# Kernel tuning notes

Hardware: AMD Instinct MI355X
Metric: run time of the kernel (lower is better)

The kernel has to match this reference:

```python
import jax, jax.numpy as jnp
import numpy as np

HEADS_FEAT = 8
HEADS_SAMP = 8
EPS = 1e-5


def _ln(x, g, b):
    m = jnp.mean(x, -1, keepdims=True)
    v = jnp.mean((x - m) ** 2, -1, keepdims=True)
    return (x - m) * jax.lax.rsqrt(v + EPS) * g + b


def _mha(q, k, v, heads, Wq, bq, Wk, bk, Wv, bv, Wo, bo, bias=None):
    # q: (N, Lq, D), k/v: (N, Lk, D); torch nn.MultiheadAttention math (eval, dropout=0)
    N, Lq, D = q.shape
    Lk = k.shape[1]
    dh = D // heads
    qh = (jnp.einsum('nld,ed->nle', q, Wq) + bq).reshape(N, Lq, heads, dh).transpose(0, 2, 1, 3)
    kh = (jnp.einsum('nld,ed->nle', k, Wk) + bk).reshape(N, Lk, heads, dh).transpose(0, 2, 1, 3)
    vh = (jnp.einsum('nld,ed->nle', v, Wv) + bv).reshape(N, Lk, heads, dh).transpose(0, 2, 1, 3)
    s = jnp.einsum('nhqd,nhkd->nhqk', qh, kh) * (dh ** -0.5)
    if bias is not None:
        s = s + bias  # bias broadcasts over heads
    a = jax.nn.softmax(s, axis=-1)
    o = jnp.einsum('nhqk,nhkd->nhqd', a, vh).transpose(0, 2, 1, 3).reshape(N, Lq, D)
    return jnp.einsum('nld,ed->nle', o, Wo) + bo


def setup_inputs() -> dict:
    key = jax.random.key(0)
    B, S, F, D = 4, 512, 32, 256
    H = 4 * D
    ks = iter(jax.random.split(key, 64))
    p = {}
    p['x'] = jax.random.normal(next(ks), (B, S, F, D), jnp.float32)
    m = jax.random.bernoulli(next(ks), 0.5, (B, F, F))
    p['attn_mask'] = m | jnp.eye(F, dtype=bool)  # diagonal True avoids fully-masked rows
    p['N_train'] = 384
    p['N_test'] = 128
    def W(shape):
        return jax.random.normal(next(ks), shape, jnp.float32) * 0.02
    for sfx in ('f', 't', 's'):
        for nm in ('Wq', 'Wk', 'Wv', 'Wo'):
            p[nm + '_' + sfx] = W((D, D))
        for nm in ('bq', 'bk', 'bv', 'bo'):
            p[nm + '_' + sfx] = jnp.zeros((D,), jnp.float32)
    for sfx in ('f', 't', 's', 'm'):
        p['g_' + sfx] = jnp.ones((D,), jnp.float32)
        p['b_' + sfx] = jnp.zeros((D,), jnp.float32)
    p['W1'] = W((H, D)); p['b1'] = jnp.zeros((H,), jnp.float32)
    p['Wg'] = W((H, D)); p['bg'] = jnp.zeros((H,), jnp.float32)
    p['W2'] = W((D, H)); p['b2'] = jnp.zeros((D,), jnp.float32)
    return p


def reference(x, attn_mask, N_train, N_test,
              Wq_f, bq_f, Wk_f, bk_f, Wv_f, bv_f, Wo_f, bo_f,
              Wq_t, bq_t, Wk_t, bk_t, Wv_t, bv_t, Wo_t, bo_t,
              Wq_s, bq_s, Wk_s, bk_s, Wv_s, bv_s, Wo_s, bo_s,
              g_f, b_f, g_t, b_t, g_s, b_s, g_m, b_m,
              W1, b1, Wg, bg, W2, b2):
    B, S, F, D = x.shape
    # --- graph-masked feature attention over F (rows = B*S) ---
    x_row = x.reshape(B * S, F, D)
    x_norm = _ln(x_row, g_f, b_f)
    bias = jnp.where(attn_mask, 0.0, -jnp.inf).astype(x.dtype)  # (B,F,F)
    bias = jnp.broadcast_to(bias[:, None, None], (B, S, 1, F, F)).reshape(B * S, 1, F, F)
    x2 = _mha(x_norm, x_norm, x_norm, HEADS_FEAT, Wq_f, bq_f, Wk_f, bk_f, Wv_f, bv_f, Wo_f, bo_f, bias)
    x_row = x_row + x2
    # --- sample attention over S (columns = B*F) ---
    x_col = x_row.reshape(B, S, F, D).transpose(0, 2, 1, 3).reshape(B * F, S, D)
    x_tr = x_col[:, :N_train]
    x_te = x_col[:, N_train:]
    x_trn = _ln(x_tr, g_t, b_t)
    x_tr = x_tr + _mha(x_trn, x_trn, x_trn, HEADS_SAMP, Wq_t, bq_t, Wk_t, bk_t, Wv_t, bv_t, Wo_t, bo_t)
    if N_test > 0:
        x_ten = _ln(x_te, g_s, b_s)
        kvn = _ln(x_tr, g_s, b_s)
        x_te = x_te + _mha(x_ten, kvn, kvn, HEADS_SAMP, Wq_s, bq_s, Wk_s, bk_s, Wv_s, bv_s, Wo_s, bo_s)
    xc = jnp.concatenate([x_tr, x_te], axis=1).reshape(B, F, S, D).transpose(0, 2, 1, 3)
    # --- SwiGLU MLP ---
    xn = _ln(xc, g_m, b_m)
    h = (jnp.einsum('bsfd,ed->bsfe', xn, W1) + b1) * jax.nn.silu(jnp.einsum('bsfd,ed->bsfe', xn, Wg) + bg)
    x2 = jnp.einsum('bsfe,de->bsfd', h, W2) + b2
    return xc + x2
```

## Files before the change

kernel.cpp:

```cpp
#include <hip/hip_runtime.h>

typedef unsigned short u16;
typedef __attribute__((ext_vector_type(8))) short short8;
typedef __attribute__((ext_vector_type(4))) float f32x4;

#define SCALE_QK 0.17677669529663687f
#define LOG2E 1.44269504088896f

__device__ __forceinline__ u16 f2b(float f) {
  union { float f; unsigned int i; } v; v.f = f;
  unsigned int x = v.i;
  x += 0x7fffu + ((x >> 16) & 1u);
  return (u16)(x >> 16);
}
__device__ __forceinline__ float lo16(unsigned int u) {
  union { unsigned int i; float f; } v; v.i = u << 16; return v.f;
}
__device__ __forceinline__ float hi16(unsigned int u) {
  union { unsigned int i; float f; } v; v.i = u & 0xffff0000u; return v.f;
}
__device__ __forceinline__ void gll16(const void* g, void* l) {
  __builtin_amdgcn_global_load_lds(
      (const __attribute__((address_space(1))) unsigned int*)g,
      (__attribute__((address_space(3))) unsigned int*)l, 16, 0, 0);
}

__device__ __forceinline__ size_t map_off(int m, int map) {
  if (map == 0) return ((size_t)m) << 8;
  int r, s;
  if (map == 1) { r = m / 384; s = m - r * 384; }
  else          { r = m >> 7;  s = 384 + (m & 127); }
  int b = r >> 5, f = r & 31;
  return ((size_t)((b * 512 + s) * 32 + f)) << 8;
}

__global__ void decode_mask_kernel(const int* __restrict__ mraw,
                                   float* __restrict__ bias) {
  __shared__ int isbyte;
  if (threadIdx.x == 0) isbyte = 0;
  __syncthreads();
  for (int i = threadIdx.x; i < 1024; i += 256) {
    unsigned int v = (unsigned int)mraw[i];
    if (v > 1u) atomicOr(&isbyte, 1);
  }
  __syncthreads();
  bool byt = (isbyte != 0);
  const unsigned char* mb = (const unsigned char*)mraw;
  for (int i = threadIdx.x; i < 4096; i += 256) {
    bool on = byt ? (mb[i] != 0) : (mraw[i] != 0);
    bias[i] = on ? 0.f : -1e30f;
  }
}

struct WPtrs { const float* p[15]; };
__global__ __launch_bounds__(256) void cvt_w_kernel(WPtrs wp, u16* __restrict__ out) {
  int gid = blockIdx.x * 256 + threadIdx.x;
  int e0 = gid * 8;
  if (e0 >= 1572864) return;
  int mi, off;
  if (e0 < 786432) { mi = e0 >> 16; off = e0 & 65535; }
  else { int j = e0 - 786432; mi = 12 + (j >> 18); off = j & 262143; }
  const float* s = wp.p[mi] + off;
  float4 a = *(const float4*)s;
  float4 b = *(const float4*)(s + 4);
  union { u16 u[8]; uint4 v; } pk;
  pk.u[0] = f2b(a.x); pk.u[1] = f2b(a.y); pk.u[2] = f2b(a.z); pk.u[3] = f2b(a.w);
  pk.u[4] = f2b(b.x); pk.u[5] = f2b(b.y); pk.u[6] = f2b(b.z); pk.u[7] = f2b(b.w);
  *(uint4*)(out + e0) = pk.v;
}

__global__ __launch_bounds__(256) void ln_kernel(
    const float* __restrict__ src, float* __restrict__ cpy,
    u16* __restrict__ dst, const float* __restrict__ g,
    const float* __restrict__ bt, int M, int map) {
  int widx = blockIdx.x * 4 + (threadIdx.x >> 6);
  if (widx >= M) return;
  int lane = threadIdx.x & 63;
  size_t off = map_off(widx, map);
  float4 xv = ((const float4*)(src + off))[lane];
  float s = xv.x + xv.y + xv.z + xv.w;
#pragma unroll
  for (int o = 32; o; o >>= 1) s += __shfl_xor(s, o);
  float mean = s * (1.f / 256.f);
  float dx = xv.x - mean, dy = xv.y - mean, dz = xv.z - mean, dw = xv.w - mean;
  float ss = dx * dx + dy * dy + dz * dz + dw * dw;
#pragma unroll
  for (int o = 32; o; o >>= 1) ss += __shfl_xor(ss, o);
  float rs = rsqrtf(ss * (1.f / 256.f) + 1e-5f);
  float4 gv = ((const float4*)g)[lane];
  float4 bv = ((const float4*)bt)[lane];
  ushort4 st;
  st.x = f2b(dx * rs * gv.x + bv.x);
  st.y = f2b(dy * rs * gv.y + bv.y);
  st.z = f2b(dz * rs * gv.z + bv.z);
  st.w = f2b(dw * rs * gv.w + bv.w);
  *(ushort4*)(dst + ((size_t)widx << 8) + lane * 4) = st;
  if (cpy) ((float4*)(cpy + off))[lane] = xv;
}

__global__ __launch_bounds__(256, 2) void gemm_nt(
    const u16* __restrict__ A, const u16* __restrict__ W,
    const float* __restrict__ bias, u16* __restrict__ outB,
    float* __restrict__ outF, int M, int N, int K, int mode) {
  __shared__ u16 As[128 * 64];
  __shared__ u16 Bs[128 * 64];
  int tid = threadIdx.x, lane = tid & 63, w = tid >> 6;
  int wr = w >> 1, wc = w & 1;
  int m0 = blockIdx.x * 128, n0 = blockIdx.y * 128;
  int fr = lane & 15, fg = lane >> 4;
  f32x4 z = {0.f, 0.f, 0.f, 0.f};
  f32x4 acc[4][4];
#pragma unroll
  for (int i = 0; i < 4; ++i)
#pragma unroll
    for (int j = 0; j < 4; ++j) acc[i][j] = z;
  int r8 = lane >> 3, seg = lane & 7;
  const u16* gA = A + (size_t)(m0 + w * 32 + r8) * K + seg * 8;
  const u16* gB = W + (size_t)(n0 + w * 32 + r8) * K + seg * 8;
  u16* lA = As + (w * 32) * 64;
  u16* lB = Bs + (w * 32) * 64;
  for (int kt = 0; kt < K; kt += 64) {
#pragma unroll
    for (int j = 0; j < 4; ++j) {
      gll16(gA + (size_t)(j * 8) * K + kt, lA + j * 512);
      gll16(gB + (size_t)(j * 8) * K + kt, lB + j * 512);
    }
    __syncthreads();
#pragma unroll
    for (int ks = 0; ks < 2; ++ks) {
      short8 af[4], bf[4];
#pragma unroll
      for (int i = 0; i < 4; ++i) {
        af[i] = *(const short8*)(As + (wr * 64 + i * 16 + fr) * 64 + ks * 32 + fg * 8);
        bf[i] = *(const short8*)(Bs + (wc * 64 + i * 16 + fr) * 64 + ks * 32 + fg * 8);
      }
#pragma unroll
      for (int mi = 0; mi < 4; ++mi)
#pragma unroll
        for (int ni = 0; ni < 4; ++ni)
          acc[mi][ni] = __builtin_amdgcn_mfma_f32_16x16x32_bf16(af[mi], bf[ni], acc[mi][ni], 0, 0, 0);
    }
    __syncthreads();
  }
#pragma unroll
  for (int mi = 0; mi < 4; ++mi)
#pragma unroll
    for (int ni = 0; ni < 4; ++ni) {
      int col = n0 + wc * 64 + ni * 16 + fr;
      float bv = bias ? bias[col] : 0.f;
#pragma unroll
      for (int r = 0; r < 4; ++r) {
        int row = m0 + wr * 64 + mi * 16 + fg * 4 + r;
        float v = acc[mi][ni][r] + bv;
        if (mode == 0) {
          outB[(size_t)row * N + col] = f2b(v);
        } else {
          outF[map_off(row, mode - 1) + col] += v;
        }
      }
    }
}

__global__ __launch_bounds__(256, 2) void gemm_dual(
    const u16* __restrict__ A, const u16* __restrict__ W1,
    const float* __restrict__ b1, const u16* __restrict__ Wg,
    const float* __restrict__ bg, u16* __restrict__ Hb,
    int M, int N, int K) {
  __shared__ u16 As[128 * 64];
  __shared__ u16 W1s[128 * 64];
  __shared__ u16 Wgs[128 * 64];
  int tid = threadIdx.x, lane = tid & 63, w = tid >> 6;
  int wr = w >> 1, wc = w & 1;
  int m0 = blockIdx.x * 128, n0 = blockIdx.y * 128;
  int fr = lane & 15, fg = lane >> 4;
  f32x4 z = {0.f, 0.f, 0.f, 0.f};
  f32x4 ac1[4][4], ac2[4][4];
#pragma unroll
  for (int i = 0; i < 4; ++i)
#pragma unroll
    for (int j = 0; j < 4; ++j) { ac1[i][j] = z; ac2[i][j] = z; }
  int r8 = lane >> 3, seg = lane & 7;
  const u16* gA = A + (size_t)(m0 + w * 32 + r8) * K + seg * 8;
  const u16* g1 = W1 + (size_t)(n0 + w * 32 + r8) * K + seg * 8;
  const u16* g2 = Wg + (size_t)(n0 + w * 32 + r8) * K + seg * 8;
  u16* lA = As + (w * 32) * 64;
  u16* l1 = W1s + (w * 32) * 64;
  u16* l2 = Wgs + (w * 32) * 64;
  for (int kt = 0; kt < K; kt += 64) {
#pragma unroll
    for (int j = 0; j < 4; ++j) {
      gll16(gA + (size_t)(j * 8) * K + kt, lA + j * 512);
      gll16(g1 + (size_t)(j * 8) * K + kt, l1 + j * 512);
      gll16(g2 + (size_t)(j * 8) * K + kt, l2 + j * 512);
    }
    __syncthreads();
#pragma unroll
    for (int ks = 0; ks < 2; ++ks) {
      short8 af[4], bf1[4], bf2[4];
#pragma unroll
      for (int i = 0; i < 4; ++i) {
        af[i]  = *(const short8*)(As  + (wr * 64 + i * 16 + fr) * 64 + ks * 32 + fg * 8);
        bf1[i] = *(const short8*)(W1s + (wc * 64 + i * 16 + fr) * 64 + ks * 32 + fg * 8);
        bf2[i] = *(const short8*)(Wgs + (wc * 64 + i * 16 + fr) * 64 + ks * 32 + fg * 8);
      }
#pragma unroll
      for (int mi = 0; mi < 4; ++mi)
#pragma unroll
        for (int ni = 0; ni < 4; ++ni) {
          ac1[mi][ni] = __builtin_amdgcn_mfma_f32_16x16x32_bf16(af[mi], bf1[ni], ac1[mi][ni], 0, 0, 0);
          ac2[mi][ni] = __builtin_amdgcn_mfma_f32_16x16x32_bf16(af[mi], bf2[ni], ac2[mi][ni], 0, 0, 0);
        }
    }
    __syncthreads();
  }
#pragma unroll
  for (int mi = 0; mi < 4; ++mi)
#pragma unroll
    for (int ni = 0; ni < 4; ++ni) {
      int col = n0 + wc * 64 + ni * 16 + fr;
      float bb1 = b1[col], bbg = bg[col];
#pragma unroll
      for (int r = 0; r < 4; ++r) {
        int row = m0 + wr * 64 + mi * 16 + fg * 4 + r;
        float v1 = ac1[mi][ni][r] + bb1;
        float v2 = ac2[mi][ni][r] + bbg;
        float sg = v2 / (1.f + __expf(-v2));
        Hb[(size_t)row * N + col] = f2b(v1 * sg);
      }
    }
}

__global__ __launch_bounds__(256) void fa_kernel(
    const u16* __restrict__ Q, const u16* __restrict__ K,
    const u16* __restrict__ V, u16* __restrict__ CTX,
    const float* __restrict__ bias) {
  __shared__ u16 Ks[8192];
  __shared__ u16 Vs[8192];
  __shared__ float Bs[1056];
  int tid = threadIdx.x;
  int row = blockIdx.x;
  size_t base = (size_t)row << 13;
#pragma unroll
  for (int it = 0; it < 4; ++it) {
    int c = it * 256 + tid;
    int tok = c >> 5, d8 = c & 31;
    int dst = ((d8 >> 2) * 32 + tok) * 32 + (d8 & 3) * 8;
    *(uint4*)&Ks[dst] = *(const uint4*)(K + base + tok * 256 + d8 * 8);
    *(uint4*)&Vs[dst] = *(const uint4*)(V + base + tok * 256 + d8 * 8);
  }
  {
    const float* bp = bias + (size_t)(row >> 9) * 1024;
#pragma unroll
    for (int it = 0; it < 4; ++it) {
      int i = it * 256 + tid;
      Bs[(i >> 5) * 33 + (i & 31)] = bp[i];
    }
  }
  __syncthreads();
  int h = tid >> 5, q = tid & 31;
  float qr[32];
  {
    const u16* qp = Q + base + q * 256 + h * 32;
    const float sc = SCALE_QK * LOG2E;
#pragma unroll
    for (int j = 0; j < 4; ++j) {
      uint4 u = ((const uint4*)qp)[j];
      qr[j * 8 + 0] = lo16(u.x) * sc; qr[j * 8 + 1] = hi16(u.x) * sc;
      qr[j * 8 + 2] = lo16(u.y) * sc; qr[j * 8 + 3] = hi16(u.y) * sc;
      qr[j * 8 + 4] = lo16(u.z) * sc; qr[j * 8 + 5] = hi16(u.z) * sc;
      qr[j * 8 + 6] = lo16(u.w) * sc; qr[j * 8 + 7] = hi16(u.w) * sc;
    }
  }
  float s[32], m = -3e38f;
  const u16* kb = Ks + h * 1024;
  const float* brow = Bs + q * 33;
#pragma unroll 4
  for (int k = 0; k < 32; ++k) {
    const uint4* kr = (const uint4*)(kb + k * 32);
    float d0 = 0.f, d1 = 0.f, d2 = 0.f, d3 = 0.f;
#pragma unroll
    for (int j = 0; j < 4; ++j) {
      uint4 u = kr[j];
      d0 += qr[j * 8 + 0] * lo16(u.x); d1 += qr[j * 8 + 1] * hi16(u.x);
      d2 += qr[j * 8 + 2] * lo16(u.y); d3 += qr[j * 8 + 3] * hi16(u.y);
      d0 += qr[j * 8 + 4] * lo16(u.z); d1 += qr[j * 8 + 5] * hi16(u.z);
      d2 += qr[j * 8 + 6] * lo16(u.w); d3 += qr[j * 8 + 7] * hi16(u.w);
    }
    float sv = (d0 + d1) + (d2 + d3) + brow[k];
    s[k] = sv;
    m = fmaxf(m, sv);
  }
  float l = 0.f;
#pragma unroll
  for (int k = 0; k < 32; ++k) {
    float p = exp2f(s[k] - m);
    s[k] = p; l += p;
  }
  float inv = 1.f / l;
  float out[32];
#pragma unroll
  for (int d = 0; d < 32; ++d) out[d] = 0.f;
  const u16* vb = Vs + h * 1024;
#pragma unroll 4
  for (int k = 0; k < 32; ++k) {
    float wgt = s[k];
    const uint4* vr = (const uint4*)(vb + k * 32);
#pragma unroll
    for (int j = 0; j < 4; ++j) {
      uint4 u = vr[j];
      out[j * 8 + 0] += wgt * lo16(u.x); out[j * 8 + 1] += wgt * hi16(u.x);
      out[j * 8 + 2] += wgt * lo16(u.y); out[j * 8 + 3] += wgt * hi16(u.y);
      out[j * 8 + 4] += wgt * lo16(u.z); out[j * 8 + 5] += wgt * hi16(u.z);
      out[j * 8 + 6] += wgt * lo16(u.w); out[j * 8 + 7] += wgt * hi16(u.w);
    }
  }
  u16* op = CTX + base + q * 256 + h * 32;
#pragma unroll
  for (int j = 0; j < 4; ++j) {
    union { u16 u[8]; uint4 v; } pk;
#pragma unroll
    for (int e = 0; e < 8; ++e) pk.u[e] = f2b(out[j * 8 + e] * inv);
    ((uint4*)op)[j] = pk.v;
  }
}

__global__ __launch_bounds__(256) void sa_mfma_kernel(
    const u16* __restrict__ Q, const u16* __restrict__ K,
    const u16* __restrict__ V, u16* __restrict__ CTX, int Lq) {
  __shared__ u16 Ks[384 * 40];
  __shared__ u16 Vt[32 * 392];
  __shared__ u16 Pb[4][16 * 72];
  int tid = threadIdx.x, lane = tid & 63, w = tid >> 6;
  int rh = blockIdx.x;
  int row = rh >> 3, h = rh & 7;
  size_t kvb = ((size_t)row * 384) * 256 + h * 32;
  for (int c = tid; c < 1536; c += 256) {
    int k = c >> 2, seg = c & 3;
    uint4 kk = *(const uint4*)(K + kvb + (size_t)k * 256 + seg * 8);
    *(uint4*)&Ks[k * 40 + seg * 8] = kk;
    uint4 vv = *(const uint4*)(V + kvb + (size_t)k * 256 + seg * 8);
    union { u16 u[8]; uint4 v; } t; t.v = vv;
#pragma unroll
    for (int j = 0; j < 8; ++j) Vt[(seg * 8 + j) * 392 + k] = t.u[j];
  }
  __syncthreads();
  int fr = lane & 15, fg = lane >> 4;
  const float sc = SCALE_QK * LOG2E;
  int nqt = Lq >> 4;
  f32x4 zz = {0.f, 0.f, 0.f, 0.f};
  for (int qt = w; qt < nqt; qt += 4) {
    int q0 = qt << 4;
    short8 a_q = *(const short8*)(Q + ((size_t)row * Lq + q0 + fr) * 256 + h * 32 + fg * 8);
    f32x4 O0 = zz, O1 = zz;
    float m[4] = {-3e38f, -3e38f, -3e38f, -3e38f};
    float l[4] = {0.f, 0.f, 0.f, 0.f};
    u16* pb = Pb[w];
    for (int c0 = 0; c0 < 384; c0 += 64) {
      f32x4 s[4];
#pragma unroll
      for (int kt = 0; kt < 4; ++kt) {
        short8 b_k = *(const short8*)(Ks + (c0 + kt * 16 + fr) * 40 + fg * 8);
        s[kt] = __builtin_amdgcn_mfma_f32_16x16x32_bf16(a_q, b_k, zz, 0, 0, 0);
      }
      float rm[4];
#pragma unroll
      for (int r = 0; r < 4; ++r)
        rm[r] = fmaxf(fmaxf(s[0][r], s[1][r]), fmaxf(s[2][r], s[3][r]));
#pragma unroll
      for (int o = 1; o <= 8; o <<= 1)
#pragma unroll
        for (int r = 0; r < 4; ++r) rm[r] = fmaxf(rm[r], __shfl_xor(rm[r], o));
      float al[4];
#pragma unroll
      for (int r = 0; r < 4; ++r) {
        float mn = fmaxf(m[r], rm[r] * sc);
        al[r] = exp2f(m[r] - mn);
        m[r] = mn;
        l[r] *= al[r];
        O0[r] *= al[r];
        O1[r] *= al[r];
      }
#pragma unroll
      for (int kt = 0; kt < 4; ++kt)
#pragma unroll
        for (int r = 0; r < 4; ++r) {
          float p = exp2f(fmaf(s[kt][r], sc, -m[r]));
          l[r] += p;
          pb[(fg * 4 + r) * 72 + kt * 16 + fr] = f2b(p);
        }
      asm volatile("s_waitcnt lgkmcnt(0)" ::: "memory");
      __builtin_amdgcn_wave_barrier();
#pragma unroll
      for (int sub = 0; sub < 2; ++sub) {
        short8 a_p = *(const short8*)(pb + fr * 72 + sub * 32 + fg * 8);
        short8 b_v0 = *(const short8*)(Vt + fr * 392 + c0 + sub * 32 + fg * 8);
        short8 b_v1 = *(const short8*)(Vt + (16 + fr) * 392 + c0 + sub * 32 + fg * 8);
        O0 = __builtin_amdgcn_mfma_f32_16x16x32_bf16(a_p, b_v0, O0, 0, 0, 0);
        O1 = __builtin_amdgcn_mfma_f32_16x16x32_bf16(a_p, b_v1, O1, 0, 0, 0);
      }
      __builtin_amdgcn_wave_barrier();
    }
#pragma unroll
    for (int o = 1; o <= 8; o <<= 1)
#pragma unroll
      for (int r = 0; r < 4; ++r) l[r] += __shfl_xor(l[r], o);
    u16* op = CTX + ((size_t)row * Lq + q0) * 256 + h * 32;
#pragma unroll
    for (int r = 0; r < 4; ++r) {
      float inv = 1.f / l[r];
      int orow = fg * 4 + r;
      op[orow * 256 + fr] = f2b(O0[r] * inv);
      op[orow * 256 + 16 + fr] = f2b(O1[r] * inv);
    }
  }
}

extern "C" void kernel_launch(void* const* d_in, const int* in_sizes, int n_in,
                              void* d_out, int out_size, void* d_ws, size_t ws_size,
                              hipStream_t stream) {
  const float* x    = (const float*)d_in[0];
  const int*   mask = (const int*)d_in[1];
  const float* bq_f = (const float*)d_in[8],  *bk_f = (const float*)d_in[9];
  const float* bv_f = (const float*)d_in[10], *bo_f = (const float*)d_in[11];
  const float* bq_t = (const float*)d_in[16], *bk_t = (const float*)d_in[17];
  const float* bv_t = (const float*)d_in[18], *bo_t = (const float*)d_in[19];
  const float* bq_s = (const float*)d_in[24], *bk_s = (const float*)d_in[25];
  const float* bv_s = (const float*)d_in[26], *bo_s = (const float*)d_in[27];
  const float* g_f = (const float*)d_in[28], *b_f = (const float*)d_in[29];
  const float* g_t = (const float*)d_in[30], *b_t = (const float*)d_in[31];
  const float* g_s = (const float*)d_in[32], *b_s = (const float*)d_in[33];
  const float* g_m = (const float*)d_in[34], *b_m = (const float*)d_in[35];
  const float* b1 = (const float*)d_in[37];
  const float* bg = (const float*)d_in[39];
  const float* b2 = (const float*)d_in[41];

  float* XR = (float*)d_out;
  char* ws = (char*)d_ws;
  float* BIAS = (float*)ws;
  u16* XN = (u16*)(ws + 16384);
  u16* QB = XN + 16777216;
  u16* KB = QB + 16777216;
  u16* VB = KB + 16777216;
  u16* XM = VB + 16777216;
  u16* WB = XM + 16777216;
  u16* HB = XN;

  WPtrs wp;
  wp.p[0] = (const float*)d_in[4];  wp.p[1] = (const float*)d_in[5];
  wp.p[2] = (const float*)d_in[6];  wp.p[3] = (const float*)d_in[7];
  wp.p[4] = (const float*)d_in[12]; wp.p[5] = (const float*)d_in[13];
  wp.p[6] = (const float*)d_in[14]; wp.p[7] = (const float*)d_in[15];
  wp.p[8] = (const float*)d_in[20]; wp.p[9] = (const float*)d_in[21];
  wp.p[10] = (const float*)d_in[22]; wp.p[11] = (const float*)d_in[23];
  wp.p[12] = (const float*)d_in[36]; wp.p[13] = (const float*)d_in[38];
  wp.p[14] = (const float*)d_in[40];
  const u16 *WQF = WB, *WKF = WB + 65536, *WVF = WB + 131072, *WOF = WB + 196608;
  const u16 *WQT = WB + 262144, *WKT = WB + 327680, *WVT = WB + 393216, *WOT = WB + 458752;
  const u16 *WQS = WB + 524288, *WKS = WB + 589824, *WVS = WB + 655360, *WOS = WB + 720896;
  const u16 *W1B = WB + 786432, *WGB = WB + 1048576, *W2B = WB + 1310720;

  cvt_w_kernel<<<768, 256, 0, stream>>>(wp, WB);
  decode_mask_kernel<<<1, 256, 0, stream>>>(mask, BIAS);

  ln_kernel<<<16384, 256, 0, stream>>>(x, XR, XN, g_f, b_f, 65536, 0);
  gemm_nt<<<dim3(512, 2), 256, 0, stream>>>(XN, WQF, bq_f, QB, nullptr, 65536, 256, 256, 0);
  gemm_nt<<<dim3(512, 2), 256, 0, stream>>>(XN, WKF, bk_f, KB, nullptr, 65536, 256, 256, 0);
  gemm_nt<<<dim3(512, 2), 256, 0, stream>>>(XN, WVF, bv_f, VB, nullptr, 65536, 256, 256, 0);
  fa_kernel<<<2048, 256, 0, stream>>>(QB, KB, VB, XN, BIAS);
  gemm_nt<<<dim3(512, 2), 256, 0, stream>>>(XN, WOF, bo_f, nullptr, XR, 65536, 256, 256, 1);

  ln_kernel<<<12288, 256, 0, stream>>>(XR, nullptr, XN, g_t, b_t, 49152, 1);
  gemm_nt<<<dim3(384, 2), 256, 0, stream>>>(XN, WQT, bq_t, QB, nullptr, 49152, 256, 256, 0);
  gemm_nt<<<dim3(384, 2), 256, 0, stream>>>(XN, WKT, bk_t, KB, nullptr, 49152, 256, 256, 0);
  gemm_nt<<<dim3(384, 2), 256, 0, stream>>>(XN, WVT, bv_t, VB, nullptr, 49152, 256, 256, 0);
  sa_mfma_kernel<<<1024, 256, 0, stream>>>(QB, KB, VB, XN, 384);
  gemm_nt<<<dim3(384, 2), 256, 0, stream>>>(XN, WOT, bo_t, nullptr, XR, 49152, 256, 256, 2);

  ln_kernel<<<4096, 256, 0, stream>>>(XR, nullptr, XN, g_s, b_s, 16384, 2);
  gemm_nt<<<dim3(128, 2), 256, 0, stream>>>(XN, WQS, bq_s, QB, nullptr, 16384, 256, 256, 0);
  ln_kernel<<<12288, 256, 0, stream>>>(XR, nullptr, XN, g_s, b_s, 49152, 1);
  gemm_nt<<<dim3(384, 2), 256, 0, stream>>>(XN, WKS, bk_s, KB, nullptr, 49152, 256, 256, 0);
  gemm_nt<<<dim3(384, 2), 256, 0, stream>>>(XN, WVS, bv_s, VB, nullptr, 49152, 256, 256, 0);
  sa_mfma_kernel<<<1024, 256, 0, stream>>>(QB, KB, VB, XN, 128);
  gemm_nt<<<dim3(128, 2), 256, 0, stream>>>(XN, WOS, bo_s, nullptr, XR, 16384, 256, 256, 3);

  ln_kernel<<<16384, 256, 0, stream>>>(XR, nullptr, XM, g_m, b_m, 65536, 0);
  gemm_dual<<<dim3(512, 8), 256, 0, stream>>>(XM, W1B, b1, WGB, bg, HB, 65536, 1024, 256);
  gemm_nt<<<dim3(512, 2), 256, 0, stream>>>(HB, W2B, b2, nullptr, XR, 65536, 256, 1024, 1);
}
```

Baseline: 1.063 ms.

## Fuse Q/K/V projections into one GEMM and XOR-swizzle LDS tiles

```diff
diff --git a/kernel.cpp b/kernel.cpp
--- a/kernel.cpp
+++ b/kernel.cpp
@@ -6,6 +6,7 @@
 
 #define SCALE_QK 0.17677669529663687f
 #define LOG2E 1.44269504088896f
+#define QKV_SPACING 16777216ULL
 
 __device__ __forceinline__ u16 f2b(float f) {
   union { float f; unsigned int i; } v; v.f = f;
@@ -100,7 +101,8 @@
 
 __global__ __launch_bounds__(256, 2) void gemm_nt(
     const u16* __restrict__ A, const u16* __restrict__ W,
-    const float* __restrict__ bias, u16* __restrict__ outB,
+    const float* __restrict__ b0, const float* __restrict__ b1,
+    const float* __restrict__ b2, u16* __restrict__ outB,
     float* __restrict__ outF, int M, int N, int K, int mode) {
   __shared__ u16 As[128 * 64];
   __shared__ u16 Bs[128 * 64];
@@ -115,8 +117,8 @@
 #pragma unroll
     for (int j = 0; j < 4; ++j) acc[i][j] = z;
   int r8 = lane >> 3, seg = lane & 7;
-  const u16* gA = A + (size_t)(m0 + w * 32 + r8) * K + seg * 8;
-  const u16* gB = W + (size_t)(n0 + w * 32 + r8) * K + seg * 8;
+  const u16* gA = A + (size_t)(m0 + w * 32 + r8) * K + (seg ^ r8) * 8;
+  const u16* gB = W + (size_t)(n0 + w * 32 + r8) * K + (seg ^ r8) * 8;
   u16* lA = As + (w * 32) * 64;
   u16* lB = Bs + (w * 32) * 64;
   for (int kt = 0; kt < K; kt += 64) {
@@ -131,8 +133,11 @@
       short8 af[4], bf[4];
 #pragma unroll
       for (int i = 0; i < 4; ++i) {
-        af[i] = *(const short8*)(As + (wr * 64 + i * 16 + fr) * 64 + ks * 32 + fg * 8);
-        bf[i] = *(const short8*)(Bs + (wc * 64 + i * 16 + fr) * 64 + ks * 32 + fg * 8);
+        int ra = wr * 64 + i * 16 + fr;
+        int rb = wc * 64 + i * 16 + fr;
+        int sw = ((ks * 4 + fg) ^ (fr & 7)) * 8;
+        af[i] = *(const short8*)(As + ra * 64 + sw);
+        bf[i] = *(const short8*)(Bs + rb * 64 + sw);
       }
 #pragma unroll
       for (int mi = 0; mi < 4; ++mi)
@@ -147,13 +152,15 @@
 #pragma unroll
     for (int ni = 0; ni < 4; ++ni) {
       int col = n0 + wc * 64 + ni * 16 + fr;
-      float bv = bias ? bias[col] : 0.f;
+      int bsel = col >> 8;
+      const float* bp = bsel == 0 ? b0 : (bsel == 1 ? b1 : b2);
+      float bv = bp ? bp[col & 255] : 0.f;
 #pragma unroll
       for (int r = 0; r < 4; ++r) {
         int row = m0 + wr * 64 + mi * 16 + fg * 4 + r;
         float v = acc[mi][ni][r] + bv;
         if (mode == 0) {
-          outB[(size_t)row * N + col] = f2b(v);
+          outB[(size_t)bsel * QKV_SPACING + (size_t)row * 256 + (col & 255)] = f2b(v);
         } else {
           outF[map_off(row, mode - 1) + col] += v;
         }
@@ -180,9 +187,9 @@
 #pragma unroll
     for (int j = 0; j < 4; ++j) { ac1[i][j] = z; ac2[i][j] = z; }
   int r8 = lane >> 3, seg = lane & 7;
-  const u16* gA = A + (size_t)(m0 + w * 32 + r8) * K + seg * 8;
-  const u16* g1 = W1 + (size_t)(n0 + w * 32 + r8) * K + seg * 8;
-  const u16* g2 = Wg + (size_t)(n0 + w * 32 + r8) * K + seg * 8;
+  const u16* gA = A + (size_t)(m0 + w * 32 + r8) * K + (seg ^ r8) * 8;
+  const u16* g1 = W1 + (size_t)(n0 + w * 32 + r8) * K + (seg ^ r8) * 8;
+  const u16* g2 = Wg + (size_t)(n0 + w * 32 + r8) * K + (seg ^ r8) * 8;
   u16* lA = As + (w * 32) * 64;
   u16* l1 = W1s + (w * 32) * 64;
   u16* l2 = Wgs + (w * 32) * 64;
@@ -199,9 +206,12 @@
       short8 af[4], bf1[4], bf2[4];
 #pragma unroll
       for (int i = 0; i < 4; ++i) {
-        af[i]  = *(const short8*)(As  + (wr * 64 + i * 16 + fr) * 64 + ks * 32 + fg * 8);
-        bf1[i] = *(const short8*)(W1s + (wc * 64 + i * 16 + fr) * 64 + ks * 32 + fg * 8);
-        bf2[i] = *(const short8*)(Wgs + (wc * 64 + i * 16 + fr) * 64 + ks * 32 + fg * 8);
+        int ra = wr * 64 + i * 16 + fr;
+        int rb = wc * 64 + i * 16 + fr;
+        int sw = ((ks * 4 + fg) ^ (fr & 7)) * 8;
+        af[i]  = *(const short8*)(As  + ra * 64 + sw);
+        bf1[i] = *(const short8*)(W1s + rb * 64 + sw);
+        bf2[i] = *(const short8*)(Wgs + rb * 64 + sw);
       }
 #pragma unroll
       for (int mi = 0; mi < 4; ++mi)
@@ -454,37 +464,36 @@
   wp.p[10] = (const float*)d_in[22]; wp.p[11] = (const float*)d_in[23];
   wp.p[12] = (const float*)d_in[36]; wp.p[13] = (const float*)d_in[38];
   wp.p[14] = (const float*)d_in[40];
-  const u16 *WQF = WB, *WKF = WB + 65536, *WVF = WB + 131072, *WOF = WB + 196608;
-  const u16 *WQT = WB + 262144, *WKT = WB + 327680, *WVT = WB + 393216, *WOT = WB + 458752;
-  const u16 *WQS = WB + 524288, *WKS = WB + 589824, *WVS = WB + 655360, *WOS = WB + 720896;
+  const u16 *WQKV_F = WB;
+  const u16 *WOF = WB + 196608;
+  const u16 *WQKV_T = WB + 262144;
+  const u16 *WOT = WB + 458752;
+  const u16 *WQS = WB + 524288;
+  const u16 *WKV_S = WB + 589824;
+  const u16 *WOS = WB + 720896;
   const u16 *W1B = WB + 786432, *WGB = WB + 1048576, *W2B = WB + 1310720;
 
   cvt_w_kernel<<<768, 256, 0, stream>>>(wp, WB);
   decode_mask_kernel<<<1, 256, 0, stream>>>(mask, BIAS);
 
   ln_kernel<<<16384, 256, 0, stream>>>(x, XR, XN, g_f, b_f, 65536, 0);
-  gemm_nt<<<dim3(512, 2), 256, 0, stream>>>(XN, WQF, bq_f, QB, nullptr, 65536, 256, 256, 0);
-  gemm_nt<<<dim3(512, 2), 256, 0, stream>>>(XN, WKF, bk_f, KB, nullptr, 65536, 256, 256, 0);
-  gemm_nt<<<dim3(512, 2), 256, 0, stream>>>(XN, WVF, bv_f, VB, nullptr, 65536, 256, 256, 0);
+  gemm_nt<<<dim3(512, 6), 256, 0, stream>>>(XN, WQKV_F, bq_f, bk_f, bv_f, QB, nullptr, 65536, 768, 256, 0);
   fa_kernel<<<2048, 256, 0, stream>>>(QB, KB, VB, XN, BIAS);
-  gemm_nt<<<dim3(512, 2), 256, 0, stream>>>(XN, WOF, bo_f, nullptr, XR, 65536, 256, 256, 1);
+  gemm_nt<<<dim3(512, 2), 256, 0, stream>>>(XN, WOF, bo_f, nullptr, nullptr, nullptr, XR, 65536, 256, 256, 1);
 
   ln_kernel<<<12288, 256, 0, stream>>>(XR, nullptr, XN, g_t, b_t, 49152, 1);
-  gemm_nt<<<dim3(384, 2), 256, 0, stream>>>(XN, WQT, bq_t, QB, nullptr, 49152, 256, 256, 0);
-  gemm_nt<<<dim3(384, 2), 256, 0, stream>>>(XN, WKT, bk_t, KB, nullptr, 49152, 256, 256, 0);
-  gemm_nt<<<dim3(384, 2), 256, 0, stream>>>(XN, WVT, bv_t, VB, nullptr, 49152, 256, 256, 0);
+  gemm_nt<<<dim3(384, 6), 256, 0, stream>>>(XN, WQKV_T, bq_t, bk_t, bv_t, QB, nullptr, 49152, 768, 256, 0);
   sa_mfma_kernel<<<1024, 256, 0, stream>>>(QB, KB, VB, XN, 384);
-  gemm_nt<<<dim3(384, 2), 256, 0, stream>>>(XN, WOT, bo_t, nullptr, XR, 49152, 256, 256, 2);
+  gemm_nt<<<dim3(384, 2), 256, 0, stream>>>(XN, WOT, bo_t, nullptr, nullptr, nullptr, XR, 49152, 256, 256, 2);
 
   ln_kernel<<<4096, 256, 0, stream>>>(XR, nullptr, XN, g_s, b_s, 16384, 2);
-  gemm_nt<<<dim3(128, 2), 256, 0, stream>>>(XN, WQS, bq_s, QB, nullptr, 16384, 256, 256, 0);
+  gemm_nt<<<dim3(128, 2), 256, 0, stream>>>(XN, WQS, bq_s, nullptr, nullptr, QB, nullptr, 16384, 256, 256, 0);
   ln_kernel<<<12288, 256, 0, stream>>>(XR, nullptr, XN, g_s, b_s, 49152, 1);
-  gemm_nt<<<dim3(384, 2), 256, 0, stream>>>(XN, WKS, bk_s, KB, nullptr, 49152, 256, 256, 0);
-  gemm_nt<<<dim3(384, 2), 256, 0, stream>>>(XN, WVS, bv_s, VB, nullptr, 49152, 256, 256, 0);
+  gemm_nt<<<dim3(384, 4), 256, 0, stream>>>(XN, WKV_S, bk_s, bv_s, nullptr, KB, nullptr, 49152, 512, 256, 0);
   sa_mfma_kernel<<<1024, 256, 0, stream>>>(QB, KB, VB, XN, 128);
-  gemm_nt<<<dim3(128, 2), 256, 0, stream>>>(XN, WOS, bo_s, nullptr, XR, 16384, 256, 256, 3);
+  gemm_nt<<<dim3(128, 2), 256, 0, stream>>>(XN, WOS, bo_s, nullptr, nullptr, nullptr, XR, 16384, 256, 256, 3);
 
   ln_kernel<<<16384, 256, 0, stream>>>(XR, nullptr, XM, g_m, b_m, 65536, 0);
   gemm_dual<<<dim3(512, 8), 256, 0, stream>>>(XM, W1B, b1, WGB, bg, HB, 65536, 1024, 256);
-  gemm_nt<<<dim3(512, 2), 256, 0, stream>>>(HB, W2B, b2, nullptr, XR, 65536, 256, 1024, 1);
-}
+  gemm_nt<<<dim3(512, 2), 256, 0, stream>>>(HB, W2B, b2, nullptr, nullptr, nullptr, XR, 65536, 256, 1024, 1);
+}
```

New measurement: 973.1 us. 1.09x faster.
